# Kernel tuning notes

Measured on AMD Instinct MI355X. Metric: run time of the kernel, lower is better.

## Reference

```python
import jax, jax.numpy as jnp
import numpy as np

B, D, H, E, TOP_K = 16384, 256, 1024, 8, 2


def setup_inputs() -> dict:
    key = jax.random.key(0)
    ks = jax.random.split(key, 12)
    s = 0.02
    return {
        "t": jax.random.uniform(ks[0], (B,), dtype=jnp.float32),
        "x": jax.random.normal(ks[1], (B, D), dtype=jnp.float32),
        # router: Linear(D+1,H) -> SiLU -> Linear(H,E)
        "Rw1": jax.random.normal(ks[2], (D + 1, H), dtype=jnp.float32) * s,
        "Rb1": jnp.zeros((H,), dtype=jnp.float32),
        "Rw2": jax.random.normal(ks[3], (H, E), dtype=jnp.float32) * s,
        "Rb2": jnp.zeros((E,), dtype=jnp.float32),
        # stacked expert MLPs: (D+1)->H->H->D for each of E experts
        "Ew1": jax.random.normal(ks[4], (E, D + 1, H), dtype=jnp.float32) * s,
        "Eb1": jnp.zeros((E, H), dtype=jnp.float32),
        "Ew2": jax.random.normal(ks[5], (E, H, H), dtype=jnp.float32) * s,
        "Eb2": jnp.zeros((E, H), dtype=jnp.float32),
        "Ew3": jax.random.normal(ks[6], (E, H, D), dtype=jnp.float32) * s,
        "Eb3": jnp.zeros((E, D), dtype=jnp.float32),
    }


def reference(t, x, Rw1, Rb1, Rw2, Rb2, Ew1, Eb1, Ew2, Eb2, Ew3, Eb3):
    t_vec = t.reshape(-1, 1)                      # (B,1)
    xt = jnp.concatenate([x, t_vec], axis=-1)     # (B,D+1)

    # router logits
    h = jax.nn.silu(xt @ Rw1 + Rb1)
    logits = h @ Rw2 + Rb2                        # (B,E)

    # top-k sparse gating (top_k < num_experts)
    topk_vals, topk_idx = jax.lax.top_k(logits, TOP_K)
    mask = jnp.zeros_like(logits).at[jnp.arange(logits.shape[0])[:, None], topk_idx].set(1.0)
    masked_logits = jnp.where(mask == 0, -jnp.inf, logits)
    alpha = jax.nn.softmax(masked_logits, axis=-1)  # (B,E)

    # dense all-expert MLPs (faithful to the original stack+einsum)
    h1 = jax.nn.silu(jnp.einsum('bi,eih->beh', xt, Ew1) + Eb1)   # (B,E,H)
    h2 = jax.nn.silu(jnp.einsum('beh,ehg->beg', h1, Ew2) + Eb2)  # (B,E,H)
    expert_out = jnp.einsum('beh,ehd->bed', h2, Ew3) + Eb3       # (B,E,D)

    velocity = jnp.einsum('be,bed->bd', alpha, expert_out)       # (B,D)
    return velocity
```

## Files before the change

### kernel.cpp

```cpp
#include <hip/hip_runtime.h>
#include <cstdint>
#include <cstddef>

#define NB   16384
#define DD   256
#define DIN  257
#define KP1  288
#define HH   1024
#define NE   8
#define GMAX 33792
#define GMT  264

#define CTRL_INTS 272

typedef unsigned short u16;
typedef __bf16 bf16x8 __attribute__((ext_vector_type(8)));
typedef float  f32x4  __attribute__((ext_vector_type(4)));

__device__ __forceinline__ u16 f2bf(float f) {
  union { float f; unsigned u; } v; v.f = f;
  return (u16)((v.u + 0x7FFFu + ((v.u >> 16) & 1u)) >> 16);
}
__device__ __forceinline__ float bf2f(u16 h) {
  union { unsigned u; float f; } v; v.u = ((unsigned)h) << 16;
  return v.f;
}

#define GLDS16(g, l) __builtin_amdgcn_global_load_lds( \
    (const __attribute__((address_space(1))) void*)(g), \
    (__attribute__((address_space(3))) void*)(l), 16, 0, 0)

__global__ void build_xt3(const float* __restrict__ x, const float* __restrict__ t,
                          u16* __restrict__ xh, u16* __restrict__ xm, u16* __restrict__ xl) {
  long i = (long)blockIdx.x * blockDim.x + threadIdx.x;
  if (i >= (long)NB * KP1) return;
  int b = (int)(i / KP1), k = (int)(i % KP1);
  float v = (k < DD) ? x[(long)b * DD + k] : (k == DD ? t[b] : 0.f);
  u16 hi = f2bf(v);  float r1 = v - bf2f(hi);
  u16 mi = f2bf(r1); float r2 = r1 - bf2f(mi);
  xh[i] = hi; xm[i] = mi; xl[i] = f2bf(r2);
}

__global__ void transpose_w(const float* __restrict__ W, u16* __restrict__ Wh,
                            u16* __restrict__ Wm, u16* __restrict__ Wl,
                            int Kdim, int Ndim, int Kpad, long sW, long sWt) {
  __shared__ float tile[32][33];
  int e = blockIdx.z;
  int k0 = blockIdx.x * 32, n0 = blockIdx.y * 32;
  int tx = threadIdx.x, ty = threadIdx.y;
  const float* Wb = W + (long)e * sW;
  #pragma unroll
  for (int i = 0; i < 4; ++i) {
    int k = k0 + ty + i * 8;
    tile[ty + i * 8][tx] = (k < Kdim) ? Wb[(long)k * Ndim + (n0 + tx)] : 0.f;
  }
  __syncthreads();
  #pragma unroll
  for (int i = 0; i < 4; ++i) {
    int n = n0 + ty + i * 8;
    float v = tile[tx][ty + i * 8];
    long o = (long)e * sWt + (long)n * Kpad + k0 + tx;
    u16 hi = f2bf(v);
    Wh[o] = hi;
    if (Wm) {
      float r1 = v - bf2f(hi);
      u16 mi = f2bf(r1);
      Wm[o] = mi;
      Wl[o] = f2bf(r1 - bf2f(mi));
    }
  }
}

__global__ __launch_bounds__(256, 2)
void router_gemm_emul3(const u16* __restrict__ Ah, const u16* __restrict__ Am, const u16* __restrict__ Al,
                       const u16* __restrict__ Bh, const u16* __restrict__ Bm, const u16* __restrict__ Bl,
                       const float* __restrict__ bias, float* __restrict__ hout) {
  __shared__ __align__(16) u16 S[6][128 * 32];
  int tid = threadIdx.x;
  int m0 = blockIdx.y * 128, n0 = blockIdx.x * 128;
  const u16* Ap[3] = {Ah, Am, Al};
  const u16* Bp[3] = {Bh, Bm, Bl};
  const u16 *ag[3][2], *bg[3][2];
  u16 *la[3][2], *lb[3][2];
  #pragma unroll
  for (int r = 0; r < 2; ++r) {
    int i = r * 256 + tid;
    int row = i >> 2, kq = (i & 3) * 8;
    #pragma unroll
    for (int p = 0; p < 3; ++p) {
      ag[p][r] = Ap[p] + (long)(m0 + row) * KP1 + kq;
      bg[p][r] = Bp[p] + (long)(n0 + row) * KP1 + kq;
      la[p][r] = &S[p][i * 8];
      lb[p][r] = &S[3 + p][i * 8];
    }
  }
  int lane = tid & 63, wv = tid >> 6;
  int wm = wv >> 1, wn = wv & 1;
  int q = lane >> 4, c = lane & 15;
  f32x4 acc[4][4];
  #pragma unroll
  for (int mi = 0; mi < 4; ++mi)
    #pragma unroll
    for (int ni = 0; ni < 4; ++ni) acc[mi][ni] = (f32x4){0.f, 0.f, 0.f, 0.f};

  for (int k0 = 0; k0 < KP1; k0 += 32) {
    __syncthreads();
    #pragma unroll
    for (int r = 0; r < 2; ++r)
      #pragma unroll
      for (int p = 0; p < 3; ++p) {
        GLDS16(ag[p][r] + k0, la[p][r]);
        GLDS16(bg[p][r] + k0, lb[p][r]);
      }
    __syncthreads();
    bf16x8 av[3][4], bv[3][4];
    #pragma unroll
    for (int mi = 0; mi < 4; ++mi) {
      int off = (wm * 64 + mi * 16 + c) * 32 + q * 8;
      #pragma unroll
      for (int p = 0; p < 3; ++p) av[p][mi] = *(const bf16x8*)&S[p][off];
    }
    #pragma unroll
    for (int ni = 0; ni < 4; ++ni) {
      int off = (wn * 64 + ni * 16 + c) * 32 + q * 8;
      #pragma unroll
      for (int p = 0; p < 3; ++p) bv[p][ni] = *(const bf16x8*)&S[3 + p][off];
    }
    #pragma unroll
    for (int mi = 0; mi < 4; ++mi)
      #pragma unroll
      for (int ni = 0; ni < 4; ++ni) {
        acc[mi][ni] = __builtin_amdgcn_mfma_f32_16x16x32_bf16(av[0][mi], bv[0][ni], acc[mi][ni], 0, 0, 0);
        acc[mi][ni] = __builtin_amdgcn_mfma_f32_16x16x32_bf16(av[0][mi], bv[1][ni], acc[mi][ni], 0, 0, 0);
        acc[mi][ni] = __builtin_amdgcn_mfma_f32_16x16x32_bf16(av[1][mi], bv[0][ni], acc[mi][ni], 0, 0, 0);
        acc[mi][ni] = __builtin_amdgcn_mfma_f32_16x16x32_bf16(av[0][mi], bv[2][ni], acc[mi][ni], 0, 0, 0);
        acc[mi][ni] = __builtin_amdgcn_mfma_f32_16x16x32_bf16(av[2][mi], bv[0][ni], acc[mi][ni], 0, 0, 0);
      }
  }
  #pragma unroll
  for (int mi = 0; mi < 4; ++mi)
    #pragma unroll
    for (int r = 0; r < 4; ++r) {
      int row = m0 + wm * 64 + mi * 16 + q * 4 + r;
      #pragma unroll
      for (int ni = 0; ni < 4; ++ni) {
        int col = n0 + wn * 64 + ni * 16 + c;
        float v = acc[mi][ni][r] + bias[col];
        v = v / (1.f + expf(-v));
        hout[(long)row * HH + col] = v;
      }
    }
}

__global__ __launch_bounds__(256)
void router_logits(const float* __restrict__ h, const float* __restrict__ Rw2,
                   const float* __restrict__ Rb2, int* __restrict__ tk_idx,
                   float* __restrict__ tk_alpha, int* __restrict__ ctrl) {
  __shared__ float wt[NE][HH];
  __shared__ int lh[NE];
  int tid = threadIdx.x;
  if (tid < NE) lh[tid] = 0;
  #pragma unroll
  for (int it = 0; it < 8; ++it) {
    int i = it * 256 + tid;
    f32x4 v = *(const f32x4*)&Rw2[i * 4];
    int k = i >> 1, e4 = (i & 1) * 4;
    #pragma unroll
    for (int j = 0; j < 4; ++j) wt[e4 + j][k] = v[j];
  }
  __syncthreads();
  int wv = tid >> 6, lane = tid & 63;
  #pragma unroll
  for (int ti = 0; ti < 4; ++ti) {
    int token = (blockIdx.x * 4 + wv) * 4 + ti;
    const float* hrow = h + (long)token * HH;
    float hv[16];
    #pragma unroll
    for (int j = 0; j < 16; ++j) hv[j] = hrow[j * 64 + lane];
    float p[NE] = {0.f, 0.f, 0.f, 0.f, 0.f, 0.f, 0.f, 0.f};
    #pragma unroll
    for (int j = 0; j < 16; ++j) {
      int k = j * 64 + lane;
      #pragma unroll
      for (int e = 0; e < NE; ++e) p[e] += hv[j] * wt[e][k];
    }
    #pragma unroll
    for (int m = 1; m < 64; m <<= 1)
      #pragma unroll
      for (int e = 0; e < NE; ++e) p[e] += __shfl_xor(p[e], m, 64);
    if (lane == 0) {
      float v[NE];
      #pragma unroll
      for (int e = 0; e < NE; ++e) v[e] = p[e] + Rb2[e];
      int i0 = 0;
      #pragma unroll
      for (int e = 1; e < NE; ++e) if (v[e] > v[i0]) i0 = e;
      int i1 = -1;
      #pragma unroll
      for (int e = 0; e < NE; ++e) { if (e == i0) continue; if (i1 < 0 || v[e] > v[i1]) i1 = e; }
      float d  = v[i1] - v[i0];
      float e1 = expf(d);
      float a0 = 1.f / (1.f + e1);
      float a1 = e1 / (1.f + e1);
      tk_idx[token * 2]     = i0;  tk_idx[token * 2 + 1]   = i1;
      tk_alpha[token * 2]   = a0;  tk_alpha[token * 2 + 1] = a1;
      atomicAdd(&lh[i0], 1);  atomicAdd(&lh[i1], 1);
    }
  }
  __syncthreads();
  if (tid < NE) atomicAdd(&ctrl[tid * 16], lh[tid]);
}

__global__ void compute_offsets(int* __restrict__ ctrl) {
  if (threadIdx.x == 0 && blockIdx.x == 0) {
    int total = 0;
    for (int e = 0; e < NE; ++e) {
      ctrl[256 + e] = total;
      total += (ctrl[e * 16] + 127) & ~127;
    }
    ctrl[256 + NE] = total;
  }
}

__global__ void build_rowmap(const int* __restrict__ tk_idx, int* __restrict__ ctrl,
                             int* __restrict__ grow, int* __restrict__ tok2slot) {
  __shared__ int lh[NE];
  __shared__ int gb[NE];
  int tid = threadIdx.x;
  if (tid < NE) lh[tid] = 0;
  __syncthreads();
  int token = blockIdx.x * 256 + tid;
  int e0 = tk_idx[token * 2], e1 = tk_idx[token * 2 + 1];
  int l0 = atomicAdd(&lh[e0], 1);
  int l1 = atomicAdd(&lh[e1], 1);
  __syncthreads();
  if (tid < NE) gb[tid] = atomicAdd(&ctrl[128 + tid * 16], lh[tid]);
  __syncthreads();
  int g0 = ctrl[256 + e0] + gb[e0] + l0;
  int g1 = ctrl[256 + e1] + gb[e1] + l1;
  grow[g0] = token;  grow[g1] = token;
  tok2slot[token * 2] = g0;  tok2slot[token * 2 + 1] = g1;
}

template<bool GATHER, bool SILU, bool OUTF32>
__global__ __launch_bounds__(256, 2)
void gemm_grouped(const u16* __restrict__ A, int lda,
                  const u16* __restrict__ Wt, long wstride, int ldw,
                  const float* __restrict__ bias, int bstride,
                  u16* __restrict__ C, int ldc,
                  float* __restrict__ Out, int ldo,
                  const int* __restrict__ offp,
                  const int* __restrict__ grow,
                  int K) {
  int m0 = blockIdx.y * 128, n0 = blockIdx.x * 128;
  if (m0 >= offp[NE]) return;
  int e = 0;
  while (m0 >= offp[e + 1]) ++e;
  __shared__ __align__(16) u16 As[128 * 32];
  __shared__ __align__(16) u16 Bs[128 * 32];
  int tid = threadIdx.x;
  const u16 *ag[2], *bg[2];
  u16 *la[2], *lb[2];
  #pragma unroll
  for (int r = 0; r < 2; ++r) {
    int i = r * 256 + tid;
    int row = i >> 2, kq = (i & 3) * 8;
    long arow = m0 + row;
    if (GATHER) arow = grow[arow];
    ag[r] = A + arow * lda + kq;
    bg[r] = Wt + (long)e * wstride + (long)(n0 + row) * ldw + kq;
    la[r] = &As[i * 8];
    lb[r] = &Bs[i * 8];
  }
  int lane = tid & 63, wv = tid >> 6;
  int wm = wv >> 1, wn = wv & 1;
  int q = lane >> 4, c = lane & 15;
  f32x4 acc[4][4];
  #pragma unroll
  for (int mi = 0; mi < 4; ++mi)
    #pragma unroll
    for (int ni = 0; ni < 4; ++ni) acc[mi][ni] = (f32x4){0.f, 0.f, 0.f, 0.f};

  for (int k0 = 0; k0 < K; k0 += 32) {
    __syncthreads();
    #pragma unroll
    for (int r = 0; r < 2; ++r) {
      GLDS16(ag[r] + k0, la[r]);
      GLDS16(bg[r] + k0, lb[r]);
    }
    __syncthreads();
    bf16x8 av[4], bv[4];
    #pragma unroll
    for (int mi = 0; mi < 4; ++mi)
      av[mi] = *(const bf16x8*)&As[(wm * 64 + mi * 16 + c) * 32 + q * 8];
    #pragma unroll
    for (int ni = 0; ni < 4; ++ni)
      bv[ni] = *(const bf16x8*)&Bs[(wn * 64 + ni * 16 + c) * 32 + q * 8];
    #pragma unroll
    for (int mi = 0; mi < 4; ++mi)
      #pragma unroll
      for (int ni = 0; ni < 4; ++ni)
        acc[mi][ni] = __builtin_amdgcn_mfma_f32_16x16x32_bf16(av[mi], bv[ni], acc[mi][ni], 0, 0, 0);
  }
  #pragma unroll
  for (int mi = 0; mi < 4; ++mi)
    #pragma unroll
    for (int r = 0; r < 4; ++r) {
      int row = wm * 64 + mi * 16 + q * 4 + r;
      #pragma unroll
      for (int ni = 0; ni < 4; ++ni) {
        int col = n0 + wn * 64 + ni * 16 + c;
        float v = acc[mi][ni][r] + bias[e * bstride + col];
        if constexpr (SILU) v = v / (1.f + __expf(-v));
        if constexpr (OUTF32) {
          Out[(long)(m0 + row) * ldo + col] = v;
        } else {
          C[(long)(m0 + row) * ldc + col] = f2bf(v);
        }
      }
    }
}

__global__ void combine_out(const float* __restrict__ eo, const int* __restrict__ tok2slot,
                            const float* __restrict__ tk_alpha, float* __restrict__ out) {
  int i = blockIdx.x * 256 + threadIdx.x;
  int token = i >> 6, c4 = (i & 63) * 4;
  long s0 = tok2slot[token * 2], s1 = tok2slot[token * 2 + 1];
  float a0 = tk_alpha[token * 2], a1 = tk_alpha[token * 2 + 1];
  f32x4 v0 = *(const f32x4*)&eo[s0 * DD + c4];
  f32x4 v1 = *(const f32x4*)&eo[s1 * DD + c4];
  f32x4 r;
  #pragma unroll
  for (int j = 0; j < 4; ++j) r[j] = a0 * v0[j] + a1 * v1[j];
  *(f32x4*)&out[(long)token * DD + c4] = r;
}

extern "C" void kernel_launch(void* const* d_in, const int* in_sizes, int n_in,
                              void* d_out, int out_size, void* d_ws, size_t ws_size,
                              hipStream_t stream) {
  const float* t   = (const float*)d_in[0];
  const float* x   = (const float*)d_in[1];
  const float* Rw1 = (const float*)d_in[2];
  const float* Rb1 = (const float*)d_in[3];
  const float* Rw2 = (const float*)d_in[4];
  const float* Rb2 = (const float*)d_in[5];
  const float* Ew1 = (const float*)d_in[6];
  const float* Eb1 = (const float*)d_in[7];
  const float* Ew2 = (const float*)d_in[8];
  const float* Eb2 = (const float*)d_in[9];
  const float* Ew3 = (const float*)d_in[10];
  const float* Eb3 = (const float*)d_in[11];
  float* out = (float*)d_out;

  char* w = (char*)d_ws;
  size_t off = 0;
  auto alloc = [&](size_t bytes) { char* p = w + off; off = (off + bytes + 255) & ~(size_t)255; return p; };
  int*   ctrl     = (int*)  alloc(CTRL_INTS * 4);
  int*   grow     = (int*)  alloc((size_t)GMAX * 4);
  size_t zero_end = off;
  int*   tok2slot = (int*)  alloc((size_t)NB * 2 * 4);
  int*   tk_idx   = (int*)  alloc((size_t)NB * 2 * 4);
  float* tk_alpha = (float*)alloc((size_t)NB * 2 * 4);
  u16* xh  = (u16*)alloc((size_t)NB * KP1 * 2);
  u16* xm  = (u16*)alloc((size_t)NB * KP1 * 2);
  u16* xl  = (u16*)alloc((size_t)NB * KP1 * 2);
  u16* R1h = (u16*)alloc((size_t)HH * KP1 * 2);
  u16* R1m = (u16*)alloc((size_t)HH * KP1 * 2);
  u16* R1l = (u16*)alloc((size_t)HH * KP1 * 2);
  u16* E1t = (u16*)alloc((size_t)NE * HH * KP1 * 2);
  u16* E2t = (u16*)alloc((size_t)NE * HH * HH * 2);
  u16* E3t = (u16*)alloc((size_t)NE * DD * HH * 2);
  u16* H1  = (u16*)alloc((size_t)GMAX * HH * 2);
  u16* H2  = (u16*)alloc((size_t)GMAX * HH * 2);
  float* hf = (float*)H1;
  float* eo = (float*)H1;

  hipMemsetAsync(d_ws, 0, zero_end, stream);

  build_xt3<<<((long)NB * KP1 + 255) / 256, 256, 0, stream>>>(x, t, xh, xm, xl);
  dim3 tb(32, 8);
  transpose_w<<<dim3(KP1 / 32, HH / 32, 1),  tb, 0, stream>>>(Rw1, R1h, R1m, R1l, DIN, HH, KP1, 0, 0);
  transpose_w<<<dim3(KP1 / 32, HH / 32, NE), tb, 0, stream>>>(Ew1, E1t, nullptr, nullptr, DIN, HH, KP1, (long)DIN * HH, (long)HH * KP1);
  transpose_w<<<dim3(HH / 32, HH / 32, NE),  tb, 0, stream>>>(Ew2, E2t, nullptr, nullptr, HH, HH, HH, (long)HH * HH, (long)HH * HH);
  transpose_w<<<dim3(HH / 32, DD / 32, NE),  tb, 0, stream>>>(Ew3, E3t, nullptr, nullptr, HH, DD, HH, (long)HH * DD, (long)DD * HH);

  router_gemm_emul3<<<dim3(HH / 128, NB / 128), 256, 0, stream>>>(xh, xm, xl, R1h, R1m, R1l, Rb1, hf);
  router_logits<<<NB / 16, 256, 0, stream>>>(hf, Rw2, Rb2, tk_idx, tk_alpha, ctrl);
  compute_offsets<<<1, 64, 0, stream>>>(ctrl);
  build_rowmap<<<NB / 256, 256, 0, stream>>>(tk_idx, ctrl, grow, tok2slot);

  const int* offp = ctrl + 256;
  gemm_grouped<true, true, false><<<dim3(HH / 128, GMT), 256, 0, stream>>>(
      xh, KP1, E1t, (long)HH * KP1, KP1, Eb1, HH, H1, HH, nullptr, 0, offp, grow, KP1);
  gemm_grouped<false, true, false><<<dim3(HH / 128, GMT), 256, 0, stream>>>(
      H1, HH, E2t, (long)HH * HH, HH, Eb2, HH, H2, HH, nullptr, 0, offp, nullptr, HH);
  gemm_grouped<false, false, true><<<dim3(DD / 128, GMT), 256, 0, stream>>>(
      H2, HH, E3t, (long)DD * HH, HH, Eb3, DD, nullptr, 0, eo, DD, offp, nullptr, HH);
  combine_out<<<(NB * DD / 4) / 256, 256, 0, stream>>>(eo, tok2slot, tk_alpha, out);
}
```

Before: 467.2 us.

## Fuse router logits into router GEMM epilogue, vectorize xt build, deepen K-steps

The router GEMM epilogue now applies SiLU and multiplies by Rw2 in registers. It writes per-column-block partial logits to a small buffer, and a new reduce_topk kernel sums them before top-k selection. This avoids writing and re-reading the full fp32 hidden matrix, which is 16384x1024. build_xt3 is vectorized to handle 4 elements per thread with u16x4 stores. The grouped expert GEMMs gain an NKT template parameter so each barrier pair loads 2 K-slices, halving the number of syncs at the cost of more LDS. The partial-sum order changes the floating-point rounding of the logits slightly, which could flip top-k ties.

```diff
diff --git a/kernel.cpp b/kernel.cpp
--- a/kernel.cpp
+++ b/kernel.cpp
@@ -16,6 +16,7 @@
 typedef unsigned short u16;
 typedef __bf16 bf16x8 __attribute__((ext_vector_type(8)));
 typedef float  f32x4  __attribute__((ext_vector_type(4)));
+typedef unsigned short u16x4 __attribute__((ext_vector_type(4)));
 
 __device__ __forceinline__ u16 f2bf(float f) {
   union { float f; unsigned u; } v; v.f = f;
@@ -32,13 +33,21 @@
 
 __global__ void build_xt3(const float* __restrict__ x, const float* __restrict__ t,
                           u16* __restrict__ xh, u16* __restrict__ xm, u16* __restrict__ xl) {
-  long i = (long)blockIdx.x * blockDim.x + threadIdx.x;
-  if (i >= (long)NB * KP1) return;
-  int b = (int)(i / KP1), k = (int)(i % KP1);
-  float v = (k < DD) ? x[(long)b * DD + k] : (k == DD ? t[b] : 0.f);
-  u16 hi = f2bf(v);  float r1 = v - bf2f(hi);
-  u16 mi = f2bf(r1); float r2 = r1 - bf2f(mi);
-  xh[i] = hi; xm[i] = mi; xl[i] = f2bf(r2);
+  long i = (long)blockIdx.x * 256 + threadIdx.x;
+  int b = (int)(i / 72), qd = (int)(i % 72);
+  f32x4 v;
+  if (qd < 64)       v = *(const f32x4*)&x[(long)b * DD + qd * 4];
+  else if (qd == 64) v = (f32x4){t[b], 0.f, 0.f, 0.f};
+  else               v = (f32x4){0.f, 0.f, 0.f, 0.f};
+  u16x4 h, m, l;
+  #pragma unroll
+  for (int j = 0; j < 4; ++j) {
+    u16 hi = f2bf(v[j]);  float r1 = v[j] - bf2f(hi);
+    u16 mi = f2bf(r1);    float r2 = r1 - bf2f(mi);
+    h[j] = hi; m[j] = mi; l[j] = f2bf(r2);
+  }
+  long o = (long)b * KP1 + qd * 4;
+  *(u16x4*)&xh[o] = h;  *(u16x4*)&xm[o] = m;  *(u16x4*)&xl[o] = l;
 }
 
 __global__ void transpose_w(const float* __restrict__ W, u16* __restrict__ Wh,
@@ -74,7 +83,8 @@
 __global__ __launch_bounds__(256, 2)
 void router_gemm_emul3(const u16* __restrict__ Ah, const u16* __restrict__ Am, const u16* __restrict__ Al,
                        const u16* __restrict__ Bh, const u16* __restrict__ Bm, const u16* __restrict__ Bl,
-                       const float* __restrict__ bias, float* __restrict__ hout) {
+                       const float* __restrict__ bias, const float* __restrict__ Rw2,
+                       float* __restrict__ pbuf) {
   __shared__ __align__(16) u16 S[6][128 * 32];
   int tid = threadIdx.x;
   int m0 = blockIdx.y * 128, n0 = blockIdx.x * 128;
@@ -137,76 +147,73 @@
         acc[mi][ni] = __builtin_amdgcn_mfma_f32_16x16x32_bf16(av[2][mi], bv[0][ni], acc[mi][ni], 0, 0, 0);
       }
   }
+  float rw2f[4][8];
+  #pragma unroll
+  for (int ni = 0; ni < 4; ++ni) {
+    const float* p = Rw2 + (long)(n0 + wn * 64 + ni * 16 + c) * NE;
+    f32x4 a = *(const f32x4*)p, b2 = *(const f32x4*)(p + 4);
+    #pragma unroll
+    for (int j = 0; j < 4; ++j) { rw2f[ni][j] = a[j]; rw2f[ni][4 + j] = b2[j]; }
+  }
+  float bi[4];
+  #pragma unroll
+  for (int ni = 0; ni < 4; ++ni) bi[ni] = bias[n0 + wn * 64 + ni * 16 + c];
   #pragma unroll
   for (int mi = 0; mi < 4; ++mi)
     #pragma unroll
     for (int r = 0; r < 4; ++r) {
-      int row = m0 + wm * 64 + mi * 16 + q * 4 + r;
+      int token = m0 + wm * 64 + mi * 16 + q * 4 + r;
+      float part[8] = {0.f, 0.f, 0.f, 0.f, 0.f, 0.f, 0.f, 0.f};
       #pragma unroll
       for (int ni = 0; ni < 4; ++ni) {
-        int col = n0 + wn * 64 + ni * 16 + c;
-        float v = acc[mi][ni][r] + bias[col];
+        float v = acc[mi][ni][r] + bi[ni];
         v = v / (1.f + expf(-v));
-        hout[(long)row * HH + col] = v;
-      }
-    }
-}
-
-__global__ __launch_bounds__(256)
-void router_logits(const float* __restrict__ h, const float* __restrict__ Rw2,
-                   const float* __restrict__ Rb2, int* __restrict__ tk_idx,
-                   float* __restrict__ tk_alpha, int* __restrict__ ctrl) {
-  __shared__ float wt[NE][HH];
+        #pragma unroll
+        for (int e = 0; e < 8; ++e) part[e] += v * rw2f[ni][e];
+      }
+      #pragma unroll
+      for (int m = 1; m < 16; m <<= 1)
+        #pragma unroll
+        for (int e = 0; e < 8; ++e) part[e] += __shfl_xor(part[e], m, 64);
+      if (c == 0) {
+        float* dst = pbuf + ((long)(blockIdx.x * 2 + wn) * NB + token) * 8;
+        *(f32x4*)dst       = (f32x4){part[0], part[1], part[2], part[3]};
+        *(f32x4*)(dst + 4) = (f32x4){part[4], part[5], part[6], part[7]};
+      }
+    }
+}
+
+__global__ void reduce_topk(const float* __restrict__ pbuf, const float* __restrict__ Rb2,
+                            int* __restrict__ tk_idx, float* __restrict__ tk_alpha,
+                            int* __restrict__ ctrl) {
   __shared__ int lh[NE];
   int tid = threadIdx.x;
   if (tid < NE) lh[tid] = 0;
-  #pragma unroll
-  for (int it = 0; it < 8; ++it) {
-    int i = it * 256 + tid;
-    f32x4 v = *(const f32x4*)&Rw2[i * 4];
-    int k = i >> 1, e4 = (i & 1) * 4;
-    #pragma unroll
-    for (int j = 0; j < 4; ++j) wt[e4 + j][k] = v[j];
-  }
-  __syncthreads();
-  int wv = tid >> 6, lane = tid & 63;
-  #pragma unroll
-  for (int ti = 0; ti < 4; ++ti) {
-    int token = (blockIdx.x * 4 + wv) * 4 + ti;
-    const float* hrow = h + (long)token * HH;
-    float hv[16];
-    #pragma unroll
-    for (int j = 0; j < 16; ++j) hv[j] = hrow[j * 64 + lane];
-    float p[NE] = {0.f, 0.f, 0.f, 0.f, 0.f, 0.f, 0.f, 0.f};
-    #pragma unroll
-    for (int j = 0; j < 16; ++j) {
-      int k = j * 64 + lane;
-      #pragma unroll
-      for (int e = 0; e < NE; ++e) p[e] += hv[j] * wt[e][k];
-    }
-    #pragma unroll
-    for (int m = 1; m < 64; m <<= 1)
-      #pragma unroll
-      for (int e = 0; e < NE; ++e) p[e] += __shfl_xor(p[e], m, 64);
-    if (lane == 0) {
-      float v[NE];
-      #pragma unroll
-      for (int e = 0; e < NE; ++e) v[e] = p[e] + Rb2[e];
-      int i0 = 0;
-      #pragma unroll
-      for (int e = 1; e < NE; ++e) if (v[e] > v[i0]) i0 = e;
-      int i1 = -1;
-      #pragma unroll
-      for (int e = 0; e < NE; ++e) { if (e == i0) continue; if (i1 < 0 || v[e] > v[i1]) i1 = e; }
-      float d  = v[i1] - v[i0];
-      float e1 = expf(d);
-      float a0 = 1.f / (1.f + e1);
-      float a1 = e1 / (1.f + e1);
-      tk_idx[token * 2]     = i0;  tk_idx[token * 2 + 1]   = i1;
-      tk_alpha[token * 2]   = a0;  tk_alpha[token * 2 + 1] = a1;
-      atomicAdd(&lh[i0], 1);  atomicAdd(&lh[i1], 1);
-    }
-  }
+  __syncthreads();
+  int token = blockIdx.x * 256 + tid;
+  float v[8];
+  #pragma unroll
+  for (int e = 0; e < 8; ++e) v[e] = Rb2[e];
+  #pragma unroll
+  for (int p = 0; p < 16; ++p) {
+    const float* src = pbuf + ((long)p * NB + token) * 8;
+    f32x4 a = *(const f32x4*)src, b = *(const f32x4*)(src + 4);
+    #pragma unroll
+    for (int j = 0; j < 4; ++j) { v[j] += a[j]; v[4 + j] += b[j]; }
+  }
+  int i0 = 0;
+  #pragma unroll
+  for (int e = 1; e < NE; ++e) if (v[e] > v[i0]) i0 = e;
+  int i1 = -1;
+  #pragma unroll
+  for (int e = 0; e < NE; ++e) { if (e == i0) continue; if (i1 < 0 || v[e] > v[i1]) i1 = e; }
+  float d  = v[i1] - v[i0];
+  float e1 = expf(d);
+  float a0 = 1.f / (1.f + e1);
+  float a1 = e1 / (1.f + e1);
+  tk_idx[token * 2]     = i0;  tk_idx[token * 2 + 1]   = i1;
+  tk_alpha[token * 2]   = a0;  tk_alpha[token * 2 + 1] = a1;
+  atomicAdd(&lh[i0], 1);  atomicAdd(&lh[i1], 1);
   __syncthreads();
   if (tid < NE) atomicAdd(&ctrl[tid * 16], lh[tid]);
 }
@@ -242,7 +249,7 @@
   tok2slot[token * 2] = g0;  tok2slot[token * 2 + 1] = g1;
 }
 
-template<bool GATHER, bool SILU, bool OUTF32>
+template<int NKT, bool GATHER, bool SILU, bool OUTF32>
 __global__ __launch_bounds__(256, 2)
 void gemm_grouped(const u16* __restrict__ A, int lda,
                   const u16* __restrict__ Wt, long wstride, int ldw,
@@ -256,22 +263,24 @@
   if (m0 >= offp[NE]) return;
   int e = 0;
   while (m0 >= offp[e + 1]) ++e;
-  __shared__ __align__(16) u16 As[128 * 32];
-  __shared__ __align__(16) u16 Bs[128 * 32];
+  __shared__ __align__(16) u16 As[NKT][128 * 32];
+  __shared__ __align__(16) u16 Bs[NKT][128 * 32];
   int tid = threadIdx.x;
-  const u16 *ag[2], *bg[2];
-  u16 *la[2], *lb[2];
-  #pragma unroll
-  for (int r = 0; r < 2; ++r) {
-    int i = r * 256 + tid;
-    int row = i >> 2, kq = (i & 3) * 8;
-    long arow = m0 + row;
-    if (GATHER) arow = grow[arow];
-    ag[r] = A + arow * lda + kq;
-    bg[r] = Wt + (long)e * wstride + (long)(n0 + row) * ldw + kq;
-    la[r] = &As[i * 8];
-    lb[r] = &Bs[i * 8];
-  }
+  const u16 *ag[NKT][2], *bg[NKT][2];
+  u16 *la[NKT][2], *lb[NKT][2];
+  #pragma unroll
+  for (int s = 0; s < NKT; ++s)
+    #pragma unroll
+    for (int r = 0; r < 2; ++r) {
+      int i = r * 256 + tid;
+      int row = i >> 2, kq = (i & 3) * 8 + s * 32;
+      long arow = m0 + row;
+      if (GATHER) arow = grow[arow];
+      ag[s][r] = A + arow * lda + kq;
+      bg[s][r] = Wt + (long)e * wstride + (long)(n0 + row) * ldw + kq;
+      la[s][r] = &As[s][i * 8];
+      lb[s][r] = &Bs[s][i * 8];
+    }
   int lane = tid & 63, wv = tid >> 6;
   int wm = wv >> 1, wn = wv & 1;
   int q = lane >> 4, c = lane & 15;
@@ -281,26 +290,31 @@
     #pragma unroll
     for (int ni = 0; ni < 4; ++ni) acc[mi][ni] = (f32x4){0.f, 0.f, 0.f, 0.f};
 
-  for (int k0 = 0; k0 < K; k0 += 32) {
+  for (int k0 = 0; k0 < K; k0 += 32 * NKT) {
     __syncthreads();
     #pragma unroll
-    for (int r = 0; r < 2; ++r) {
-      GLDS16(ag[r] + k0, la[r]);
-      GLDS16(bg[r] + k0, lb[r]);
-    }
+    for (int s = 0; s < NKT; ++s)
+      #pragma unroll
+      for (int r = 0; r < 2; ++r) {
+        GLDS16(ag[s][r] + k0, la[s][r]);
+        GLDS16(bg[s][r] + k0, lb[s][r]);
+      }
     __syncthreads();
-    bf16x8 av[4], bv[4];
-    #pragma unroll
-    for (int mi = 0; mi < 4; ++mi)
-      av[mi] = *(const bf16x8*)&As[(wm * 64 + mi * 16 + c) * 32 + q * 8];
-    #pragma unroll
-    for (int ni = 0; ni < 4; ++ni)
-      bv[ni] = *(const bf16x8*)&Bs[(wn * 64 + ni * 16 + c) * 32 + q * 8];
-    #pragma unroll
-    for (int mi = 0; mi < 4; ++mi)
+    #pragma unroll
+    for (int s = 0; s < NKT; ++s) {
+      bf16x8 av[4], bv[4];
+      #pragma unroll
+      for (int mi = 0; mi < 4; ++mi)
+        av[mi] = *(const bf16x8*)&As[s][(wm * 64 + mi * 16 + c) * 32 + q * 8];
       #pragma unroll
       for (int ni = 0; ni < 4; ++ni)
-        acc[mi][ni] = __builtin_amdgcn_mfma_f32_16x16x32_bf16(av[mi], bv[ni], acc[mi][ni], 0, 0, 0);
+        bv[ni] = *(const bf16x8*)&Bs[s][(wn * 64 + ni * 16 + c) * 32 + q * 8];
+      #pragma unroll
+      for (int mi = 0; mi < 4; ++mi)
+        #pragma unroll
+        for (int ni = 0; ni < 4; ++ni)
+          acc[mi][ni] = __builtin_amdgcn_mfma_f32_16x16x32_bf16(av[mi], bv[ni], acc[mi][ni], 0, 0, 0);
+    }
   }
   #pragma unroll
   for (int mi = 0; mi < 4; ++mi)
@@ -361,6 +375,7 @@
   int*   tok2slot = (int*)  alloc((size_t)NB * 2 * 4);
   int*   tk_idx   = (int*)  alloc((size_t)NB * 2 * 4);
   float* tk_alpha = (float*)alloc((size_t)NB * 2 * 4);
+  float* pbuf     = (float*)alloc((size_t)16 * NB * 8 * 4);
   u16* xh  = (u16*)alloc((size_t)NB * KP1 * 2);
   u16* xm  = (u16*)alloc((size_t)NB * KP1 * 2);
   u16* xl  = (u16*)alloc((size_t)NB * KP1 * 2);
@@ -372,29 +387,28 @@
   u16* E3t = (u16*)alloc((size_t)NE * DD * HH * 2);
   u16* H1  = (u16*)alloc((size_t)GMAX * HH * 2);
   u16* H2  = (u16*)alloc((size_t)GMAX * HH * 2);
-  float* hf = (float*)H1;
   float* eo = (float*)H1;
 
   hipMemsetAsync(d_ws, 0, zero_end, stream);
 
-  build_xt3<<<((long)NB * KP1 + 255) / 256, 256, 0, stream>>>(x, t, xh, xm, xl);
+  build_xt3<<<(NB * 72) / 256, 256, 0, stream>>>(x, t, xh, xm, xl);
   dim3 tb(32, 8);
   transpose_w<<<dim3(KP1 / 32, HH / 32, 1),  tb, 0, stream>>>(Rw1, R1h, R1m, R1l, DIN, HH, KP1, 0, 0);
   transpose_w<<<dim3(KP1 / 32, HH / 32, NE), tb, 0, stream>>>(Ew1, E1t, nullptr, nullptr, DIN, HH, KP1, (long)DIN * HH, (long)HH * KP1);
   transpose_w<<<dim3(HH / 32, HH / 32, NE),  tb, 0, stream>>>(Ew2, E2t, nullptr, nullptr, HH, HH, HH, (long)HH * HH, (long)HH * HH);
   transpose_w<<<dim3(HH / 32, DD / 32, NE),  tb, 0, stream>>>(Ew3, E3t, nullptr, nullptr, HH, DD, HH, (long)HH * DD, (long)DD * HH);
 
-  router_gemm_emul3<<<dim3(HH / 128, NB / 128), 256, 0, stream>>>(xh, xm, xl, R1h, R1m, R1l, Rb1, hf);
-  router_logits<<<NB / 16, 256, 0, stream>>>(hf, Rw2, Rb2, tk_idx, tk_alpha, ctrl);
+  router_gemm_emul3<<<dim3(HH / 128, NB / 128), 256, 0, stream>>>(xh, xm, xl, R1h, R1m, R1l, Rb1, Rw2, pbuf);
+  reduce_topk<<<NB / 256, 256, 0, stream>>>(pbuf, Rb2, tk_idx, tk_alpha, ctrl);
   compute_offsets<<<1, 64, 0, stream>>>(ctrl);
   build_rowmap<<<NB / 256, 256, 0, stream>>>(tk_idx, ctrl, grow, tok2slot);
 
   const int* offp = ctrl + 256;
-  gemm_grouped<true, true, false><<<dim3(HH / 128, GMT), 256, 0, stream>>>(
+  gemm_grouped<1, true, true, false><<<dim3(HH / 128, GMT), 256, 0, stream>>>(
       xh, KP1, E1t, (long)HH * KP1, KP1, Eb1, HH, H1, HH, nullptr, 0, offp, grow, KP1);
-  gemm_grouped<false, true, false><<<dim3(HH / 128, GMT), 256, 0, stream>>>(
+  gemm_grouped<2, false, true, false><<<dim3(HH / 128, GMT), 256, 0, stream>>>(
       H1, HH, E2t, (long)HH * HH, HH, Eb2, HH, H2, HH, nullptr, 0, offp, nullptr, HH);
-  gemm_grouped<false, false, true><<<dim3(DD / 128, GMT), 256, 0, stream>>>(
+  gemm_grouped<2, false, false, true><<<dim3(DD / 128, GMT), 256, 0, stream>>>(
       H2, HH, E3t, (long)DD * HH, HH, Eb3, DD, nullptr, 0, eo, DD, offp, nullptr, HH);
   combine_out<<<(NB * DD / 4) / 256, 256, 0, stream>>>(eo, tok2slot, tk_alpha, out);
 }
```

Result: faster. 438.1 us (-6.2%).
